# Optimization experiments

Hardware: AMD Instinct MI355X
Metric: run time of the kernel (lower is better)

Reference implementation:

```python
import jax, jax.numpy as jnp
import numpy as np
import math

H = 80; W = 80
FOVX = math.pi / 2.0; FOVY = math.pi / 2.0
TANX = math.tan(FOVX * 0.5); TANY = math.tan(FOVY * 0.5)
FOCAL_X = W / (2.0 * TANX); FOCAL_Y = H / (2.0 * TANY)
SCALE_MOD = 1.0
N_GAUSS = 4096; K_GEOM = 1024; K_SH = 1024

SH_C0 = 0.28209479177387814
SH_C1 = 0.4886025119029199
C2 = [1.0925484305920792, -1.0925484305920792, 0.31539156525252005, -1.0925484305920792, 0.5462742152960396]
C3 = [-0.5900435899266435, 2.890611442640554, -0.4570457994644658, 0.3731763325901154, -0.4570457994644658, 1.445305721320277, -0.5900435899266435]


def eval_sh3(sh, d):
    # sh: [N,16,3], d: [N,3] unit view directions -> clamped RGB [N,3]
    x, y, z = d[:, 0:1], d[:, 1:2], d[:, 2:3]
    xx, yy, zz = x * x, y * y, z * z
    xy, yz, xz = x * y, y * z, x * z
    res = (SH_C0 * sh[:, 0]
           - SH_C1 * y * sh[:, 1] + SH_C1 * z * sh[:, 2] - SH_C1 * x * sh[:, 3]
           + C2[0] * xy * sh[:, 4] + C2[1] * yz * sh[:, 5]
           + C2[2] * (2.0 * zz - xx - yy) * sh[:, 6]
           + C2[3] * xz * sh[:, 7] + C2[4] * (xx - yy) * sh[:, 8]
           + C3[0] * y * (3.0 * xx - yy) * sh[:, 9] + C3[1] * xy * z * sh[:, 10]
           + C3[2] * y * (4.0 * zz - xx - yy) * sh[:, 11]
           + C3[3] * z * (2.0 * zz - 3.0 * xx - 3.0 * yy) * sh[:, 12]
           + C3[4] * x * (4.0 * zz - xx - yy) * sh[:, 13]
           + C3[5] * z * (xx - yy) * sh[:, 14]
           + C3[6] * x * (xx - yy - 3.0 * zz) * sh[:, 15])
    return jnp.maximum(res + 0.5, 0.0)


def quat_to_rotmat(q):
    # q: [N,4] normalized (w,x,y,z) -> [N,3,3]
    w, x, y, z = q[:, 0], q[:, 1], q[:, 2], q[:, 3]
    r0 = jnp.stack([1 - 2 * (y * y + z * z), 2 * (x * y - w * z), 2 * (x * z + w * y)], -1)
    r1 = jnp.stack([2 * (x * y + w * z), 1 - 2 * (x * x + z * z), 2 * (y * z - w * x)], -1)
    r2 = jnp.stack([2 * (x * z - w * y), 2 * (y * z + w * x), 1 - 2 * (x * x + y * y)], -1)
    return jnp.stack([r0, r1, r2], axis=1)


def _forward(means3D, sh, sh_indices, g_indices, opacities, scales, scale_factors, rotations, extrinsic, bg):
    N = means3D.shape[0]
    # row-vector convention as in the torch wrapper: p_hom = [x,y,z,1] @ view
    R3 = extrinsic[:3, :3]; t3 = extrinsic[3, :3]
    p_view = means3D @ R3 + t3  # [N,3] camera space
    tx, ty, tz = p_view[:, 0], p_view[:, 1], p_view[:, 2]
    in_front = tz > 0.2  # near-plane cull as in CUDA kernel
    tz_s = jnp.where(in_front, tz, 1.0)
    # NDC (projection matrix reduces to x/(z tanx), y/(z tany)) then ndc2Pix
    gx = ((tx / (tz_s * TANX) + 1.0) * W - 1.0) * 0.5
    gy = ((ty / (tz_s * TANY) + 1.0) * H - 1.0) * 0.5
    # indexed 3D covariance: Sigma = R diag(s^2) R^T, codebook gathers
    s = scales[g_indices] * scale_factors * SCALE_MOD  # [N,3]
    q = rotations[g_indices]
    q = q / jnp.linalg.norm(q, axis=1, keepdims=True)
    Rm = quat_to_rotmat(q)
    cov3D = jnp.einsum('nij,nj,nkj->nik', Rm, s * s, Rm)
    # EWA splat: world->cam rotation is R3^T under row-vector storage
    Wm = R3.T
    cov_cam = jnp.einsum('ij,njk,lk->nil', Wm, cov3D, Wm)
    limx = 1.3 * TANX; limy = 1.3 * TANY
    txc = jnp.clip(tx / tz_s, -limx, limx) * tz_s
    tyc = jnp.clip(ty / tz_s, -limy, limy) * tz_s
    J = jnp.zeros((N, 2, 3), means3D.dtype)
    J = J.at[:, 0, 0].set(FOCAL_X / tz_s).at[:, 0, 2].set(-FOCAL_X * txc / (tz_s * tz_s))
    J = J.at[:, 1, 1].set(FOCAL_Y / tz_s).at[:, 1, 2].set(-FOCAL_Y * tyc / (tz_s * tz_s))
    cov2d = jnp.einsum('nij,njk,nlk->nil', J, cov_cam, J)
    a = cov2d[:, 0, 0] + 0.3; b = cov2d[:, 0, 1]; c = cov2d[:, 1, 1] + 0.3
    det = a * c - b * b
    valid = in_front & (det > 0)
    det_s = jnp.where(det != 0, det, 1.0)
    ca = c / det_s; cb = -b / det_s; cc = a / det_s  # conic
    mid = 0.5 * (a + c)
    lam1 = mid + jnp.sqrt(jnp.maximum(0.1, mid * mid - det))
    radii = jnp.where(valid, jnp.ceil(3.0 * jnp.sqrt(lam1)), 0.0).astype(jnp.int32)
    # SH -> RGB, view dir from camera position (extrinsic.inverse()[3,:3])
    campos = jnp.linalg.inv(extrinsic)[3, :3]
    dirs = means3D - campos
    dirs = dirs / jnp.linalg.norm(dirs, axis=1, keepdims=True)
    color = eval_sh3(sh[sh_indices], dirs)  # [N,3]
    # global front-to-back depth sort
    depth = jnp.where(valid, tz, jnp.inf)
    order = jnp.argsort(depth)
    gx_s, gy_s = gx[order], gy[order]
    ca_s, cb_s, cc_s = ca[order], cb[order], cc[order]
    op_s = opacities[order, 0]; col_s = color[order]; val_s = valid[order]
    # pixel grid (pixel centers at integer coords as in renderCUDA)
    ys, xs = jnp.meshgrid(jnp.arange(H, dtype=means3D.dtype), jnp.arange(W, dtype=means3D.dtype), indexing='ij')
    px = xs.reshape(-1); py = ys.reshape(-1)  # [P]
    dx = gx_s[None, :] - px[:, None]  # [P,N]
    dy = gy_s[None, :] - py[:, None]
    power = -0.5 * (ca_s * dx * dx + cc_s * dy * dy) - cb_s * dx * dy
    alpha = jnp.minimum(0.99, op_s[None, :] * jnp.exp(jnp.minimum(power, 0.0)))
    keep = (power <= 0.0) & val_s[None, :] & (alpha >= 1.0 / 255.0)
    alpha = jnp.where(keep, alpha, 0.0)
    om = 1.0 - alpha
    T_inc = jnp.cumprod(om, axis=1)
    inc = T_inc >= 1e-4  # early-termination prefix (T monotone)
    T_excl = jnp.concatenate([jnp.ones((px.shape[0], 1), om.dtype), T_inc[:, :-1]], axis=1)
    w = alpha * T_excl * inc
    T_final = jnp.prod(jnp.where(inc, om, 1.0), axis=1)
    out = w @ col_s + T_final[:, None] * bg[None, :]  # [P,3]
    color_img = jnp.transpose(out.reshape(H, W, 3), (2, 0, 1))  # [3,H,W]
    return color_img, radii


def setup_inputs() -> dict:
    key = jax.random.key(0)
    ks = jax.random.split(key, 9)
    xy = (jax.random.uniform(ks[0], (N_GAUSS, 2)) - 0.5) * 4.0
    z = jax.random.uniform(ks[1], (N_GAUSS, 1)) * 4.0 + 2.0
    means3D = jnp.concatenate([xy, z], axis=1)  # inside the view frustum
    sh = jax.random.normal(ks[2], (K_SH, 16, 3)) * 0.3
    sh_indices = jax.random.randint(ks[3], (N_GAUSS,), 0, K_SH)
    g_indices = jax.random.randint(ks[4], (N_GAUSS,), 0, K_GEOM)
    opacities = jax.random.uniform(ks[5], (N_GAUSS, 1), minval=0.1, maxval=0.99)
    scales = jax.random.uniform(ks[6], (K_GEOM, 3), minval=0.01, maxval=0.08)
    scale_factors = jax.random.uniform(ks[7], (N_GAUSS, 1), minval=0.5, maxval=1.5)
    rotations = jax.random.normal(ks[8], (K_GEOM, 4))
    extrinsic = jnp.eye(4, dtype=jnp.float32)
    bg = jnp.zeros((3,), jnp.float32)
    return dict(means3D=means3D, sh=sh, sh_indices=sh_indices, g_indices=g_indices,
                opacities=opacities, scales=scales, scale_factors=scale_factors,
                rotations=rotations, extrinsic=extrinsic, bg=bg)


def reference(means3D, sh, sh_indices, g_indices, opacities, scales, scale_factors, rotations, extrinsic, bg):
    return _forward(means3D, sh, sh_indices, g_indices, opacities, scales, scale_factors, rotations, extrinsic, bg)
```

## Files before the change

kernel.cpp:

```cpp
#include <hip/hip_runtime.h>
#include <math.h>

#define NG 4096
#define WI 80
#define HI 80
#define NPIX (WI*HI)
#define FOCAL 40.0f
#define LIM 1.3f
#define CAP 1024

#define SH_C0 0.28209479177387814f
#define SH_C1 0.4886025119029199f

__global__ __launch_bounds__(256) void prep_k(
    const float* __restrict__ means, const float* __restrict__ sh,
    const int* __restrict__ shidx, const int* __restrict__ gidx,
    const float* __restrict__ opac, const float* __restrict__ scales,
    const float* __restrict__ sfac, const float* __restrict__ rots,
    const float* __restrict__ ext, float4* __restrict__ ws,
    float* __restrict__ radii_out)
{
  int i = blockIdx.x*blockDim.x + threadIdx.x;
  if (i >= NG) return;
  float e0=ext[0],  e1=ext[1],  e2=ext[2];
  float e4=ext[4],  e5=ext[5],  e6=ext[6];
  float e8=ext[8],  e9=ext[9],  e10=ext[10];
  float e12=ext[12], e13=ext[13], e14=ext[14];
  float m0=means[3*i+0], m1=means[3*i+1], m2=means[3*i+2];
  float tx = m0*e0 + m1*e4 + m2*e8  + e12;
  float ty = m0*e1 + m1*e5 + m2*e9  + e13;
  float tz = m0*e2 + m1*e6 + m2*e10 + e14;
  bool infront = tz > 0.2f;
  float tzs = infront ? tz : 1.0f;
  float inv_tzs = 1.0f / tzs;
  float gx = ((tx*inv_tzs + 1.0f)*WI - 1.0f)*0.5f;
  float gy = ((ty*inv_tzs + 1.0f)*HI - 1.0f)*0.5f;

  int gi = gidx[i];
  float sf = sfac[i];
  float s0 = scales[3*gi+0]*sf, s1 = scales[3*gi+1]*sf, s2 = scales[3*gi+2]*sf;
  float qw = rots[4*gi+0], qx = rots[4*gi+1], qy = rots[4*gi+2], qz = rots[4*gi+3];
  float qinv = rsqrtf(qw*qw+qx*qx+qy*qy+qz*qz);
  qw*=qinv; qx*=qinv; qy*=qinv; qz*=qinv;
  float r00 = 1.0f - 2.0f*(qy*qy+qz*qz);
  float r01 = 2.0f*(qx*qy - qw*qz);
  float r02 = 2.0f*(qx*qz + qw*qy);
  float r10 = 2.0f*(qx*qy + qw*qz);
  float r11 = 1.0f - 2.0f*(qx*qx+qz*qz);
  float r12 = 2.0f*(qy*qz - qw*qx);
  float r20 = 2.0f*(qx*qz - qw*qy);
  float r21 = 2.0f*(qy*qz + qw*qx);
  float r22 = 1.0f - 2.0f*(qx*qx+qy*qy);
  float v0 = s0*s0, v1 = s1*s1, v2 = s2*s2;
  float C00 = r00*r00*v0 + r01*r01*v1 + r02*r02*v2;
  float C01 = r00*r10*v0 + r01*r11*v1 + r02*r12*v2;
  float C02 = r00*r20*v0 + r01*r21*v1 + r02*r22*v2;
  float C11 = r10*r10*v0 + r11*r11*v1 + r12*r12*v2;
  float C12 = r10*r20*v0 + r11*r21*v1 + r12*r22*v2;
  float C22 = r20*r20*v0 + r21*r21*v1 + r22*r22*v2;
  float W0x=e0, W0y=e4, W0z=e8;
  float W1x=e1, W1y=e5, W1z=e9;
  float W2x=e2, W2y=e6, W2z=e10;
  float B00 = W0x*C00 + W0y*C01 + W0z*C02;
  float B01 = W0x*C01 + W0y*C11 + W0z*C12;
  float B02 = W0x*C02 + W0y*C12 + W0z*C22;
  float B10 = W1x*C00 + W1y*C01 + W1z*C02;
  float B11 = W1x*C01 + W1y*C11 + W1z*C12;
  float B12 = W1x*C02 + W1y*C12 + W1z*C22;
  float B20 = W2x*C00 + W2y*C01 + W2z*C02;
  float B21 = W2x*C01 + W2y*C11 + W2z*C12;
  float B22 = W2x*C02 + W2y*C12 + W2z*C22;
  float V00 = B00*W0x + B01*W0y + B02*W0z;
  float V01 = B00*W1x + B01*W1y + B02*W1z;
  float V02 = B00*W2x + B01*W2y + B02*W2z;
  float V11 = B10*W1x + B11*W1y + B12*W1z;
  float V12 = B10*W2x + B11*W2y + B12*W2z;
  float V22 = B20*W2x + B21*W2y + B22*W2z;
  float txz = tx*inv_tzs, tyz = ty*inv_tzs;
  float txc = fminf(fmaxf(txz, -LIM), LIM) * tzs;
  float tyc = fminf(fmaxf(tyz, -LIM), LIM) * tzs;
  float jx  = FOCAL*inv_tzs;
  float jy  = FOCAL*inv_tzs;
  float jz0 = -FOCAL*txc*inv_tzs*inv_tzs;
  float jz1 = -FOCAL*tyc*inv_tzs*inv_tzs;
  float c00 = jx*jx*V00 + 2.0f*jx*jz0*V02 + jz0*jz0*V22;
  float c01 = jx*jy*V01 + jx*jz1*V02 + jz0*jy*V12 + jz0*jz1*V22;
  float c11 = jy*jy*V11 + 2.0f*jy*jz1*V12 + jz1*jz1*V22;
  float a = c00 + 0.3f;
  float b = c01;
  float cf = c11 + 0.3f;
  float det = a*cf - b*b;
  bool valid = infront && (det > 0.0f);
  float dets = (det != 0.0f) ? det : 1.0f;
  float ca = cf/dets, cb = -b/dets, cc = a/dets;
  float mid = 0.5f*(a+cf);
  float lam1 = mid + sqrtf(fmaxf(0.1f, mid*mid - det));
  float radf = valid ? ceilf(3.0f*sqrtf(lam1)) : 0.0f;
  radii_out[i] = radf;

  float op = valid ? opac[i] : 0.0f;
  float rc = valid ? sqrtf(fmaxf(0.0f, 2.0f*logf(255.0f*op))*lam1) + 0.01f : 0.0f;

  float cp0 = -(e12*e0 + e13*e1 + e14*e2);
  float cp1 = -(e12*e4 + e13*e5 + e14*e6);
  float cp2 = -(e12*e8 + e13*e9 + e14*e10);
  float dx0 = m0-cp0, dy0 = m1-cp1, dz0 = m2-cp2;
  float dn = rsqrtf(dx0*dx0+dy0*dy0+dz0*dz0);
  float x = dx0*dn, y = dy0*dn, z = dz0*dn;
  float xx=x*x, yy=y*y, zz=z*z;
  float xy=x*y, yz=y*z, xz=x*z;
  float bf[16];
  bf[0]  = SH_C0;
  bf[1]  = -SH_C1*y;
  bf[2]  =  SH_C1*z;
  bf[3]  = -SH_C1*x;
  bf[4]  =  1.0925484305920792f*xy;
  bf[5]  = -1.0925484305920792f*yz;
  bf[6]  =  0.31539156525252005f*(2.0f*zz-xx-yy);
  bf[7]  = -1.0925484305920792f*xz;
  bf[8]  =  0.5462742152960396f*(xx-yy);
  bf[9]  = -0.5900435899266435f*y*(3.0f*xx-yy);
  bf[10] =  2.890611442640554f*xy*z;
  bf[11] = -0.4570457994644658f*y*(4.0f*zz-xx-yy);
  bf[12] =  0.3731763325901154f*z*(2.0f*zz-3.0f*xx-3.0f*yy);
  bf[13] = -0.4570457994644658f*x*(4.0f*zz-xx-yy);
  bf[14] =  1.445305721320277f*z*(xx-yy);
  bf[15] = -0.5900435899266435f*x*(xx-yy-3.0f*zz);
  const float* S = sh + (long)shidx[i]*48;
  float cr=0.f, cg=0.f, cbl=0.f;
  #pragma unroll
  for (int j=0;j<16;j++) {
    float w = bf[j];
    cr  += w*S[j*3+0];
    cg  += w*S[j*3+1];
    cbl += w*S[j*3+2];
  }
  cr  = fmaxf(cr +0.5f, 0.0f);
  cg  = fmaxf(cg +0.5f, 0.0f);
  cbl = fmaxf(cbl+0.5f, 0.0f);

  ws[i]        = make_float4(gx, gy, rc, infront ? tz : __builtin_inff());
  ws[NG + i]   = make_float4(ca, cb, cc, op);
  ws[2*NG + i] = make_float4(cr, cg, cbl, 0.0f);
}

__global__ __launch_bounds__(512) void tile_k(const float4* __restrict__ ws,
                                              const float* __restrict__ bg,
                                              float* __restrict__ out)
{
  __shared__ unsigned long long kds[CAP];
  __shared__ int   sidx[CAP];
  __shared__ float2 sgxy[CAP];
  __shared__ float4 sabc[CAP];
  __shared__ float4 scol[CAP];
  __shared__ float pT[8][64], pR[8][64], pG[8][64], pB[8][64];
  __shared__ int scnt;
  int tid = threadIdx.x;
  if (tid == 0) scnt = 0;
  __syncthreads();

  int tile = blockIdx.x;
  int x0 = (tile % 10) * 8, y0 = (tile / 10) * 8;
  float bx0 = (float)x0, bx1 = (float)(x0+7);
  float by0 = (float)y0, by1 = (float)(y0+7);

  for (int c = 0; c < NG/512; ++c) {
    int g = c*512 + tid;
    float4 v = ws[g];
    float nx = fminf(fmaxf(v.x, bx0), bx1) - v.x;
    float ny = fminf(fmaxf(v.y, by0), by1) - v.y;
    if (v.z > 0.0f && nx*nx + ny*ny <= v.z*v.z) {
      int slot = atomicAdd(&scnt, 1);
      if (slot < CAP)
        kds[slot] = ((unsigned long long)__float_as_uint(v.w) << 32) | (unsigned)g;
    }
  }
  __syncthreads();
  int cnt = scnt; if (cnt > CAP) cnt = CAP;

  for (int i = tid; i < cnt; i += 512) {
    unsigned long long ki = kds[i];
    int r = 0;
    for (int j = 0; j < cnt; ++j) r += (kds[j] < ki);
    sidx[r] = (int)(ki & 0xFFFFFFFFull);
  }
  __syncthreads();

  for (int i = tid; i < cnt; i += 512) {
    int g = sidx[i];
    float4 v = ws[g];
    sgxy[i] = make_float2(v.x, v.y);
    sabc[i] = ws[NG + g];
    scol[i] = ws[2*NG + g];
  }
  __syncthreads();

  int wv = tid >> 6, lane = tid & 63;
  float px = (float)(x0 + (lane & 7));
  float py = (float)(y0 + (lane >> 3));
  int seg = (cnt + 7) >> 3;
  int s0i = wv*seg;
  int s1i = s0i + seg; if (s1i > cnt) s1i = cnt;
  float T = 1.0f, ar = 0.f, ag = 0.f, ab = 0.f;
  for (int e = s0i; e < s1i; ++e) {
    float2 xyv = sgxy[e];
    float4 q   = sabc[e];
    float dx = xyv.x - px, dy = xyv.y - py;
    float power = -0.5f*(q.x*dx*dx + q.z*dy*dy) - q.y*dx*dy;
    float al = 0.0f;
    if (power <= 0.0f) {
      float av = fminf(0.99f, q.w*__expf(power));
      if (av >= (1.0f/255.0f)) al = av;
    }
    float4 cl = scol[e];
    float w = al*T;
    ar += w*cl.x; ag += w*cl.y; ab += w*cl.z;
    T *= 1.0f - al;
    if (__ballot(T >= 1e-4f) == 0ull) break;
  }
  pT[wv][lane]=T; pR[wv][lane]=ar; pG[wv][lane]=ag; pB[wv][lane]=ab;
  __syncthreads();

  if (tid < 64) {
    float Tg = 1.0f, r = 0.f, g2 = 0.f, b2 = 0.f;
    #pragma unroll
    for (int w = 0; w < 8; ++w) {
      r  += Tg*pR[w][tid];
      g2 += Tg*pG[w][tid];
      b2 += Tg*pB[w][tid];
      Tg *= pT[w][tid];
    }
    int p = (y0 + (tid>>3))*WI + (x0 + (tid&7));
    out[0*NPIX+p] = r  + Tg*bg[0];
    out[1*NPIX+p] = g2 + Tg*bg[1];
    out[2*NPIX+p] = b2 + Tg*bg[2];
  }
}

extern "C" void kernel_launch(void* const* d_in, const int* in_sizes, int n_in,
                              void* d_out, int out_size, void* d_ws, size_t ws_size,
                              hipStream_t stream) {
  const float* means  = (const float*)d_in[0];
  const float* sh     = (const float*)d_in[1];
  const int*   shidx  = (const int*)  d_in[2];
  const int*   gidx   = (const int*)  d_in[3];
  const float* opac   = (const float*)d_in[4];
  const float* scales = (const float*)d_in[5];
  const float* sfac   = (const float*)d_in[6];
  const float* rots   = (const float*)d_in[7];
  const float* ext    = (const float*)d_in[8];
  const float* bg     = (const float*)d_in[9];
  float* out = (float*)d_out;
  float4* ws = (float4*)d_ws;

  prep_k<<<NG/256, 256, 0, stream>>>(means, sh, shidx, gidx, opac, scales, sfac,
                                     rots, ext, ws, out + 3*NPIX);
  tile_k<<<100, 512, 0, stream>>>(ws, bg, out);
}
```

Before: 97.65 us.

## Use per-axis bounding boxes, wave-aggregated atomics, and chunked early exit in tile kernel

Replaces the circular tile-culling radius with separate x/y extents derived from the covariance diagonal, so each Gaussian is tested against the tile with an axis-aligned box. This culls more Gaussians per tile and shrinks the list to sort and blend. Slot allocation now uses one atomic per wavefront via ballot/popcount instead of one per thread. The blending loop checks for saturation only once per 16-element chunk and unrolls the inner loop; the sort loop is also unrolled. Depth moves into the colour record's spare lane, and the per-axis box changes numerics slightly versus the old radius.

```diff
diff --git a/kernel.cpp b/kernel.cpp
--- a/kernel.cpp
+++ b/kernel.cpp
@@ -99,7 +99,9 @@
   radii_out[i] = radf;
 
   float op = valid ? opac[i] : 0.0f;
-  float rc = valid ? sqrtf(fmaxf(0.0f, 2.0f*logf(255.0f*op))*lam1) + 0.01f : 0.0f;
+  float L2 = 2.0f*fmaxf(0.0f, logf(255.0f*op));
+  float rcx = valid ? sqrtf(L2*a)  + 0.01f : 0.0f;
+  float rcy = valid ? sqrtf(L2*cf) + 0.01f : 0.0f;
 
   float cp0 = -(e12*e0 + e13*e1 + e14*e2);
   float cp1 = -(e12*e4 + e13*e5 + e14*e6);
@@ -139,9 +141,9 @@
   cg  = fmaxf(cg +0.5f, 0.0f);
   cbl = fmaxf(cbl+0.5f, 0.0f);
 
-  ws[i]        = make_float4(gx, gy, rc, infront ? tz : __builtin_inff());
+  ws[i]        = make_float4(gx, gy, rcx, rcy);
   ws[NG + i]   = make_float4(ca, cb, cc, op);
-  ws[2*NG + i] = make_float4(cr, cg, cbl, 0.0f);
+  ws[2*NG + i] = make_float4(cr, cg, cbl, infront ? tz : __builtin_inff());
 }
 
 __global__ __launch_bounds__(512) void tile_k(const float4* __restrict__ ws,
@@ -149,13 +151,14 @@
                                               float* __restrict__ out)
 {
   __shared__ unsigned long long kds[CAP];
-  __shared__ int   sidx[CAP];
+  __shared__ int    sidx[CAP];
   __shared__ float2 sgxy[CAP];
   __shared__ float4 sabc[CAP];
   __shared__ float4 scol[CAP];
   __shared__ float pT[8][64], pR[8][64], pG[8][64], pB[8][64];
   __shared__ int scnt;
   int tid = threadIdx.x;
+  int wv = tid >> 6, lane = tid & 63;
   if (tid == 0) scnt = 0;
   __syncthreads();
 
@@ -164,15 +167,26 @@
   float bx0 = (float)x0, bx1 = (float)(x0+7);
   float by0 = (float)y0, by1 = (float)(y0+7);
 
+  const float* wsf = (const float*)ws;
   for (int c = 0; c < NG/512; ++c) {
     int g = c*512 + tid;
     float4 v = ws[g];
-    float nx = fminf(fmaxf(v.x, bx0), bx1) - v.x;
-    float ny = fminf(fmaxf(v.y, by0), by1) - v.y;
-    if (v.z > 0.0f && nx*nx + ny*ny <= v.z*v.z) {
-      int slot = atomicAdd(&scnt, 1);
-      if (slot < CAP)
-        kds[slot] = ((unsigned long long)__float_as_uint(v.w) << 32) | (unsigned)g;
+    bool hit = (v.z > 0.0f) &&
+               (v.x + v.z >= bx0) && (v.x - v.z <= bx1) &&
+               (v.y + v.w >= by0) && (v.y - v.w <= by1);
+    unsigned long long m = __ballot(hit);
+    if (m) {
+      int wcnt = __popcll(m);
+      int base = 0;
+      if (lane == 0) base = atomicAdd(&scnt, wcnt);
+      base = __shfl(base, 0, 64);
+      if (hit) {
+        int pos = base + __popcll(m & ((1ull<<lane)-1ull));
+        if (pos < CAP) {
+          float depth = wsf[(2*NG + g)*4 + 3];
+          kds[pos] = ((unsigned long long)__float_as_uint(depth) << 32) | (unsigned)g;
+        }
+      }
     }
   }
   __syncthreads();
@@ -181,6 +195,7 @@
   for (int i = tid; i < cnt; i += 512) {
     unsigned long long ki = kds[i];
     int r = 0;
+    #pragma unroll 8
     for (int j = 0; j < cnt; ++j) r += (kds[j] < ki);
     sidx[r] = (int)(ki & 0xFFFFFFFFull);
   }
@@ -195,28 +210,30 @@
   }
   __syncthreads();
 
-  int wv = tid >> 6, lane = tid & 63;
   float px = (float)(x0 + (lane & 7));
   float py = (float)(y0 + (lane >> 3));
   int seg = (cnt + 7) >> 3;
   int s0i = wv*seg;
   int s1i = s0i + seg; if (s1i > cnt) s1i = cnt;
   float T = 1.0f, ar = 0.f, ag = 0.f, ab = 0.f;
-  for (int e = s0i; e < s1i; ++e) {
-    float2 xyv = sgxy[e];
-    float4 q   = sabc[e];
-    float dx = xyv.x - px, dy = xyv.y - py;
-    float power = -0.5f*(q.x*dx*dx + q.z*dy*dy) - q.y*dx*dy;
-    float al = 0.0f;
-    if (power <= 0.0f) {
-      float av = fminf(0.99f, q.w*__expf(power));
-      if (av >= (1.0f/255.0f)) al = av;
+  for (int e0 = s0i; e0 < s1i && __ballot(T >= 1e-4f); e0 += 16) {
+    int e1 = e0 + 16; if (e1 > s1i) e1 = s1i;
+    #pragma unroll 4
+    for (int e = e0; e < e1; ++e) {
+      float2 xyv = sgxy[e];
+      float4 q   = sabc[e];
+      float dx = xyv.x - px, dy = xyv.y - py;
+      float power = -0.5f*(q.x*dx*dx + q.z*dy*dy) - q.y*dx*dy;
+      float al = 0.0f;
+      if (power <= 0.0f) {
+        float av = fminf(0.99f, q.w*__expf(power));
+        if (av >= (1.0f/255.0f)) al = av;
+      }
+      float4 cl = scol[e];
+      float w = al*T;
+      ar += w*cl.x; ag += w*cl.y; ab += w*cl.z;
+      T *= 1.0f - al;
     }
-    float4 cl = scol[e];
-    float w = al*T;
-    ar += w*cl.x; ag += w*cl.y; ab += w*cl.z;
-    T *= 1.0f - al;
-    if (__ballot(T >= 1e-4f) == 0ull) break;
   }
   pT[wv][lane]=T; pR[wv][lane]=ar; pG[wv][lane]=ag; pB[wv][lane]=ab;
   __syncthreads();
```

Result: faster. 93.86 us (-3.9%).
